# Performance work log

Measured on AMD Instinct MI355X. Metric: run time of the kernel, lower is better.

## Reference

```python
import jax, jax.numpy as jnp
import numpy as np

EPS = 1e-3


def setup_inputs() -> dict:
    key = jax.random.key(0)
    k1, k2 = jax.random.split(key)
    U, N, C_in, C_out = 40000, 32, 9, 64
    inputs = jax.random.normal(k1, (U, N, C_in), dtype=jnp.float32)
    # torch nn.Linear weight has shape (out, in)
    W = jax.random.normal(k2, (C_out, C_in), dtype=jnp.float32) * (1.0 / np.sqrt(C_in))
    gamma = jnp.ones((C_out,), dtype=jnp.float32)
    beta = jnp.zeros((C_out,), dtype=jnp.float32)
    return {"inputs": inputs, "W": W, "gamma": gamma, "beta": beta}


def reference(inputs, W, gamma, beta):
    # Linear (no bias): (U, N, C_in) x (C_out, C_in) -> (U, N, C_out)
    x = jnp.einsum('unc,oc->uno', inputs, W)
    # BatchNorm1d in training mode: stats over batch and points dims (U, N),
    # biased variance, as torch uses for normalization.
    mean = jnp.mean(x, axis=(0, 1))            # (C_out,)
    var = jnp.var(x, axis=(0, 1))              # (C_out,) biased
    x = (x - mean) * jax.lax.rsqrt(var + EPS) * gamma + beta
    x = jax.nn.relu(x)
    # Max over points dim, keepdim -> (U, 1, C_out)
    return jnp.max(x, axis=1, keepdims=True)
```

## Files before the change

kernel.cpp:

```cpp
#include <hip/hip_runtime.h>
#include <math.h>

#define U_TOTAL 40000
#define N_PTS   32
#define C_IN    9
#define C_OUT   64
#define UPB     8
#define NBLK_A  (U_TOTAL / UPB)
#define EPSV    1e-3f

typedef float  f32x2  __attribute__((ext_vector_type(2)));
typedef float  f32x16 __attribute__((ext_vector_type(16)));
typedef short  short8 __attribute__((ext_vector_type(8)));

__device__ __forceinline__ void gl_lds16(const void* g, void* l) {
    __builtin_amdgcn_global_load_lds(
        (const __attribute__((address_space(1))) unsigned int*)g,
        (__attribute__((address_space(3))) unsigned int*)l, 16, 0, 0);
}

__device__ __forceinline__ unsigned pk_bf16(float lo, float hi) {
    unsigned r;
    asm("v_cvt_pk_bf16_f32 %0, %1, %2" : "=v"(r) : "v"(lo), "v"(hi));
    return r;
}

__global__ __launch_bounds__(256, 4)
void pfn_a(const float* __restrict__ in, const float* __restrict__ Wg,
           float* __restrict__ out, float* __restrict__ partials)
{
    __shared__ __align__(16) float lbuf[UPB * N_PTS * C_IN];
    __shared__ float red[4][2][64];

    const int tid  = threadIdx.x;
    const int lane = tid & 63;
    const int w    = tid >> 6;
    const int col  = lane & 31;
    const int g    = lane >> 5;

    unsigned b0[4], b1[4];
    {
        const float* wr0 = Wg + (size_t)col * C_IN + g * 4;
        const float* wr1 = Wg + (size_t)(32 + col) * C_IN + g * 4;
        float a0 = wr0[0], a1 = wr0[1], a2 = wr0[2], a3 = wr0[3];
        float c0 = wr1[0], c1 = wr1[1], c2 = wr1[2], c3 = wr1[3];
        float k8a = g ? 0.f : Wg[(size_t)col * C_IN + 8];
        float k8c = g ? 0.f : Wg[(size_t)(32 + col) * C_IN + 8];
        b0[0] = pk_bf16(a0, a1); b0[1] = pk_bf16(a2, a3);
        b0[2] = pk_bf16(k8a, 0.f); b0[3] = 0u;
        b1[0] = pk_bf16(c0, c1); b1[1] = pk_bf16(c2, c3);
        b1[2] = pk_bf16(k8c, 0.f); b1[3] = 0u;
    }
    union { unsigned u[4]; short8 v; } B0, B1;
    B0.u[0]=b0[0]; B0.u[1]=b0[1]; B0.u[2]=b0[2]; B0.u[3]=b0[3];
    B1.u[0]=b1[0]; B1.u[1]=b1[1]; B1.u[2]=b1[2]; B1.u[3]=b1[3];

    const char* gt = (const char*)in + (size_t)blockIdx.x * (UPB * N_PTS * C_IN * 4);
    {
        int s0 = tid;
        gl_lds16(gt + s0 * 16, (char*)lbuf + (s0 & ~63) * 16);
        int s1 = 256 + tid;
        gl_lds16(gt + s1 * 16, (char*)lbuf + (s1 & ~63) * 16);
        if (tid < 64) {
            int s2 = 512 + tid;
            gl_lds16(gt + s2 * 16, (char*)lbuf + (s2 & ~63) * 16);
        }
    }
    __syncthreads();

    f32x2 S1_0 = {0.f,0.f}, S2_0 = {0.f,0.f}, S1_1 = {0.f,0.f}, S2_1 = {0.f,0.f};
    const int u0 = blockIdx.x * UPB;

#pragma unroll
    for (int t = 0; t < 2; ++t) {
        const int uloc = 2 * w + t;
        const int r    = uloc * N_PTS + col;
        const float* rp = lbuf + (size_t)r * C_IN;

        float f0 = rp[g * 4 + 0], f1 = rp[g * 4 + 1];
        float f2 = rp[g * 4 + 2], f3 = rp[g * 4 + 3];
        float f4 = rp[g ? 4 : 8];
        f4 = g ? 0.f : f4;
        union { unsigned u[4]; short8 v; } A;
        A.u[0] = pk_bf16(f0, f1);
        A.u[1] = pk_bf16(f2, f3);
        A.u[2] = pk_bf16(f4, 0.f);
        A.u[3] = 0u;

        f32x16 z = {};
        f32x16 d0 = __builtin_amdgcn_mfma_f32_32x32x16_bf16(A.v, B0.v, z, 0, 0, 0);
        f32x16 d1 = __builtin_amdgcn_mfma_f32_32x32x16_bf16(A.v, B1.v, z, 0, 0, 0);

        union { f32x16 v; f32x2 p[8]; } D0, D1;
        D0.v = d0; D1.v = d1;
        f32x2 mx0 = D0.p[0], mx1 = D1.p[0];
#pragma unroll
        for (int i = 0; i < 8; ++i) {
            S1_0 += D0.p[i];
            S2_0 = __builtin_elementwise_fma(D0.p[i], D0.p[i], S2_0);
            S1_1 += D1.p[i];
            S2_1 = __builtin_elementwise_fma(D1.p[i], D1.p[i], S2_1);
            if (i) {
                mx0 = __builtin_elementwise_max(mx0, D0.p[i]);
                mx1 = __builtin_elementwise_max(mx1, D1.p[i]);
            }
        }
        float m0 = fmaxf(mx0.x, mx0.y);
        float m1 = fmaxf(mx1.x, mx1.y);
        m0 = fmaxf(m0, __shfl_xor(m0, 32));
        m1 = fmaxf(m1, __shfl_xor(m1, 32));
        out[(size_t)(u0 + uloc) * C_OUT + lane] = g ? m1 : m0;
    }

    float s1_0 = S1_0.x + S1_0.y, s2_0 = S2_0.x + S2_0.y;
    float s1_1 = S1_1.x + S1_1.y, s2_1 = S2_1.x + S2_1.y;
    s1_0 += __shfl_xor(s1_0, 32);
    s2_0 += __shfl_xor(s2_0, 32);
    s1_1 += __shfl_xor(s1_1, 32);
    s2_1 += __shfl_xor(s2_1, 32);
    if (g == 0) {
        red[w][0][col]      = s1_0;
        red[w][0][32 + col] = s1_1;
        red[w][1][col]      = s2_0;
        red[w][1][32 + col] = s2_1;
    }
    __syncthreads();
    if (tid < 128) {
        const int o = tid >> 1, k = tid & 1;
        float acc = red[0][k][o] + red[1][k][o] + red[2][k][o] + red[3][k][o];
        partials[(size_t)blockIdx.x * 128 + tid] = acc;
    }
}

__global__ __launch_bounds__(256)
void pfn_reduce(const float* __restrict__ partials, float* __restrict__ sums, int nblocks)
{
    const int b = blockIdx.x;
    const int t = threadIdx.x;
    float acc = 0.f;
    for (int i = t; i < nblocks; i += 256) acc += partials[(size_t)i * 128 + b];
    __shared__ float r[256];
    r[t] = acc;
    __syncthreads();
    for (int s = 128; s > 0; s >>= 1) {
        if (t < s) r[t] += r[t + s];
        __syncthreads();
    }
    if (t == 0) sums[b] = r[0];
}

__global__ __launch_bounds__(256)
void pfn_c(float* __restrict__ out, const float* __restrict__ sums,
           const float* __restrict__ gamma, const float* __restrict__ beta)
{
    const int idx = blockIdx.x * 256 + threadIdx.x;
    const int o = (idx & 15) * 4;
    const float invM = 1.0f / (float)(U_TOTAL * N_PTS);
    float4 v   = ((const float4*)out)[idx];
    float4 s01 = ((const float4*)sums)[(2 * o) / 4];
    float4 s23 = ((const float4*)sums)[(2 * o) / 4 + 1];
    float4 g4  = ((const float4*)gamma)[o / 4];
    float4 b4  = ((const float4*)beta)[o / 4];

#define BN1(x, S1, S2, g, b) ({                                   \
        float mean_ = (S1) * invM;                                \
        float var_  = (S2) * invM - mean_ * mean_;                \
        float sc_   = (g) * __frsqrt_rn(var_ + EPSV);             \
        fmaxf(fmaf((x), sc_, (b) - mean_ * sc_), 0.0f); })

    v.x = BN1(v.x, s01.x, s01.y, g4.x, b4.x);
    v.y = BN1(v.y, s01.z, s01.w, g4.y, b4.y);
    v.z = BN1(v.z, s23.x, s23.y, g4.z, b4.z);
    v.w = BN1(v.w, s23.z, s23.w, g4.w, b4.w);
#undef BN1
    ((float4*)out)[idx] = v;
}

extern "C" void kernel_launch(void* const* d_in, const int* in_sizes, int n_in,
                              void* d_out, int out_size, void* d_ws, size_t ws_size,
                              hipStream_t stream)
{
    const float* in    = (const float*)d_in[0];
    const float* Wg    = (const float*)d_in[1];
    const float* gamma = (const float*)d_in[2];
    const float* beta  = (const float*)d_in[3];
    float* out = (float*)d_out;

    float* partials = (float*)d_ws;
    float* sums     = partials + (size_t)NBLK_A * 128;

    pfn_a<<<NBLK_A, 256, 0, stream>>>(in, Wg, out, partials);
    pfn_reduce<<<128, 256, 0, stream>>>(partials, sums, NBLK_A);
    pfn_c<<<(U_TOTAL * C_OUT / 4) / 256, 256, 0, stream>>>(out, sums, gamma, beta);
}
```

Baseline: 31.92 us.

## Double-buffer input chunks per block and transpose partials layout for coalesced reduce

Each block now processes four 8-unit chunks, staging them into two LDS buffers with async global-to-LDS loads, so loading the next chunk overlaps compute on the current one. Blocks drop from 5000 to 1250, which cuts per-block weight setup and partial count. The partials array is transposed so the reduce kernel reads contiguous addresses. The cost is explicit vmcnt waits and barriers per chunk, plus less block-level parallelism to hide latency.

```diff
diff --git a/kernel.cpp b/kernel.cpp
--- a/kernel.cpp
+++ b/kernel.cpp
@@ -5,8 +5,11 @@
 #define N_PTS   32
 #define C_IN    9
 #define C_OUT   64
-#define UPB     8
+#define UPC     8
+#define CPB     4
+#define UPB     (UPC * CPB)
 #define NBLK_A  (U_TOTAL / UPB)
+#define CHUNK_BYTES (UPC * N_PTS * C_IN * 4)
 #define EPSV    1e-3f
 
 typedef float  f32x2  __attribute__((ext_vector_type(2)));
@@ -25,11 +28,24 @@
     return r;
 }
 
+#define WAITV(N) asm volatile("s_waitcnt vmcnt(" #N ")" ::: "memory")
+
+__device__ __forceinline__ void stage_chunk(const char* __restrict__ src,
+                                            char* dst, int tid) {
+    if (tid < 192) {
+#pragma unroll
+        for (int i = 0; i < 3; ++i) {
+            const int slot = i * 192 + tid;
+            gl_lds16(src + slot * 16, dst + (slot & ~63) * 16);
+        }
+    }
+}
+
 __global__ __launch_bounds__(256, 4)
 void pfn_a(const float* __restrict__ in, const float* __restrict__ Wg,
            float* __restrict__ out, float* __restrict__ partials)
 {
-    __shared__ __align__(16) float lbuf[UPB * N_PTS * C_IN];
+    __shared__ __align__(16) float lbuf[2][UPC * N_PTS * C_IN];
     __shared__ float red[4][2][64];
 
     const int tid  = threadIdx.x;
@@ -38,7 +54,13 @@
     const int col  = lane & 31;
     const int g    = lane >> 5;
 
-    unsigned b0[4], b1[4];
+    const char* gtile = (const char*)in + (size_t)blockIdx.x * (CPB * CHUNK_BYTES);
+
+    stage_chunk(gtile + 0 * CHUNK_BYTES, (char*)lbuf[0], tid);
+    stage_chunk(gtile + 1 * CHUNK_BYTES, (char*)lbuf[1], tid);
+    __builtin_amdgcn_sched_barrier(0);
+
+    union { unsigned u[4]; short8 v; } B0, B1;
     {
         const float* wr0 = Wg + (size_t)col * C_IN + g * 4;
         const float* wr1 = Wg + (size_t)(32 + col) * C_IN + g * 4;
@@ -46,70 +68,68 @@
         float c0 = wr1[0], c1 = wr1[1], c2 = wr1[2], c3 = wr1[3];
         float k8a = g ? 0.f : Wg[(size_t)col * C_IN + 8];
         float k8c = g ? 0.f : Wg[(size_t)(32 + col) * C_IN + 8];
-        b0[0] = pk_bf16(a0, a1); b0[1] = pk_bf16(a2, a3);
-        b0[2] = pk_bf16(k8a, 0.f); b0[3] = 0u;
-        b1[0] = pk_bf16(c0, c1); b1[1] = pk_bf16(c2, c3);
-        b1[2] = pk_bf16(k8c, 0.f); b1[3] = 0u;
-    }
-    union { unsigned u[4]; short8 v; } B0, B1;
-    B0.u[0]=b0[0]; B0.u[1]=b0[1]; B0.u[2]=b0[2]; B0.u[3]=b0[3];
-    B1.u[0]=b1[0]; B1.u[1]=b1[1]; B1.u[2]=b1[2]; B1.u[3]=b1[3];
-
-    const char* gt = (const char*)in + (size_t)blockIdx.x * (UPB * N_PTS * C_IN * 4);
-    {
-        int s0 = tid;
-        gl_lds16(gt + s0 * 16, (char*)lbuf + (s0 & ~63) * 16);
-        int s1 = 256 + tid;
-        gl_lds16(gt + s1 * 16, (char*)lbuf + (s1 & ~63) * 16);
-        if (tid < 64) {
-            int s2 = 512 + tid;
-            gl_lds16(gt + s2 * 16, (char*)lbuf + (s2 & ~63) * 16);
-        }
-    }
-    __syncthreads();
+        B0.u[0] = pk_bf16(a0, a1);  B0.u[1] = pk_bf16(a2, a3);
+        B0.u[2] = pk_bf16(k8a, 0.f); B0.u[3] = 0u;
+        B1.u[0] = pk_bf16(c0, c1);  B1.u[1] = pk_bf16(c2, c3);
+        B1.u[2] = pk_bf16(k8c, 0.f); B1.u[3] = 0u;
+    }
 
     f32x2 S1_0 = {0.f,0.f}, S2_0 = {0.f,0.f}, S1_1 = {0.f,0.f}, S2_1 = {0.f,0.f};
     const int u0 = blockIdx.x * UPB;
 
 #pragma unroll
-    for (int t = 0; t < 2; ++t) {
-        const int uloc = 2 * w + t;
-        const int r    = uloc * N_PTS + col;
-        const float* rp = lbuf + (size_t)r * C_IN;
-
-        float f0 = rp[g * 4 + 0], f1 = rp[g * 4 + 1];
-        float f2 = rp[g * 4 + 2], f3 = rp[g * 4 + 3];
-        float f4 = rp[g ? 4 : 8];
-        f4 = g ? 0.f : f4;
-        union { unsigned u[4]; short8 v; } A;
-        A.u[0] = pk_bf16(f0, f1);
-        A.u[1] = pk_bf16(f2, f3);
-        A.u[2] = pk_bf16(f4, 0.f);
-        A.u[3] = 0u;
-
-        f32x16 z = {};
-        f32x16 d0 = __builtin_amdgcn_mfma_f32_32x32x16_bf16(A.v, B0.v, z, 0, 0, 0);
-        f32x16 d1 = __builtin_amdgcn_mfma_f32_32x32x16_bf16(A.v, B1.v, z, 0, 0, 0);
-
-        union { f32x16 v; f32x2 p[8]; } D0, D1;
-        D0.v = d0; D1.v = d1;
-        f32x2 mx0 = D0.p[0], mx1 = D1.p[0];
-#pragma unroll
-        for (int i = 0; i < 8; ++i) {
-            S1_0 += D0.p[i];
-            S2_0 = __builtin_elementwise_fma(D0.p[i], D0.p[i], S2_0);
-            S1_1 += D1.p[i];
-            S2_1 = __builtin_elementwise_fma(D1.p[i], D1.p[i], S2_1);
-            if (i) {
-                mx0 = __builtin_elementwise_max(mx0, D0.p[i]);
-                mx1 = __builtin_elementwise_max(mx1, D1.p[i]);
+    for (int c = 0; c < CPB; ++c) {
+        if (c < CPB - 1) { if (w < 3) WAITV(3); }
+        else             { WAITV(0); }
+        __builtin_amdgcn_s_barrier();
+        __builtin_amdgcn_sched_barrier(0);
+
+        const float* lb = lbuf[c & 1];
+#pragma unroll
+        for (int t = 0; t < 2; ++t) {
+            const int uloc = 2 * w + t;
+            const float* rp = lb + (size_t)(uloc * N_PTS + col) * C_IN;
+
+            float f0 = rp[g * 4 + 0], f1 = rp[g * 4 + 1];
+            float f2 = rp[g * 4 + 2], f3 = rp[g * 4 + 3];
+            float f4 = rp[g ? 4 : 8];
+            f4 = g ? 0.f : f4;
+            union { unsigned u[4]; short8 v; } A;
+            A.u[0] = pk_bf16(f0, f1);
+            A.u[1] = pk_bf16(f2, f3);
+            A.u[2] = pk_bf16(f4, 0.f);
+            A.u[3] = 0u;
+
+            f32x16 z = {};
+            f32x16 d0 = __builtin_amdgcn_mfma_f32_32x32x16_bf16(A.v, B0.v, z, 0, 0, 0);
+            f32x16 d1 = __builtin_amdgcn_mfma_f32_32x32x16_bf16(A.v, B1.v, z, 0, 0, 0);
+
+            union { f32x16 v; f32x2 p[8]; } D0, D1;
+            D0.v = d0; D1.v = d1;
+            f32x2 mx0 = D0.p[0], mx1 = D1.p[0];
+#pragma unroll
+            for (int i = 0; i < 8; ++i) {
+                S1_0 += D0.p[i];
+                S2_0 = __builtin_elementwise_fma(D0.p[i], D0.p[i], S2_0);
+                S1_1 += D1.p[i];
+                S2_1 = __builtin_elementwise_fma(D1.p[i], D1.p[i], S2_1);
+                if (i) {
+                    mx0 = __builtin_elementwise_max(mx0, D0.p[i]);
+                    mx1 = __builtin_elementwise_max(mx1, D1.p[i]);
+                }
             }
+            float m0 = fmaxf(mx0.x, mx0.y);
+            float m1 = fmaxf(mx1.x, mx1.y);
+            m0 = fmaxf(m0, __shfl_xor(m0, 32));
+            m1 = fmaxf(m1, __shfl_xor(m1, 32));
+            out[(size_t)(u0 + c * UPC + uloc) * C_OUT + lane] = g ? m1 : m0;
         }
-        float m0 = fmaxf(mx0.x, mx0.y);
-        float m1 = fmaxf(mx1.x, mx1.y);
-        m0 = fmaxf(m0, __shfl_xor(m0, 32));
-        m1 = fmaxf(m1, __shfl_xor(m1, 32));
-        out[(size_t)(u0 + uloc) * C_OUT + lane] = g ? m1 : m0;
+
+        __builtin_amdgcn_sched_barrier(0);
+        __builtin_amdgcn_s_barrier();
+        if (c + 2 < CPB)
+            stage_chunk(gtile + (c + 2) * CHUNK_BYTES, (char*)lbuf[c & 1], tid);
+        __builtin_amdgcn_sched_barrier(0);
     }
 
     float s1_0 = S1_0.x + S1_0.y, s2_0 = S2_0.x + S2_0.y;
@@ -128,7 +148,7 @@
     if (tid < 128) {
         const int o = tid >> 1, k = tid & 1;
         float acc = red[0][k][o] + red[1][k][o] + red[2][k][o] + red[3][k][o];
-        partials[(size_t)blockIdx.x * 128 + tid] = acc;
+        partials[(size_t)tid * NBLK_A + blockIdx.x] = acc;
     }
 }
 
@@ -138,7 +158,7 @@
     const int b = blockIdx.x;
     const int t = threadIdx.x;
     float acc = 0.f;
-    for (int i = t; i < nblocks; i += 256) acc += partials[(size_t)i * 128 + b];
+    for (int i = t; i < nblocks; i += 256) acc += partials[(size_t)b * nblocks + i];
     __shared__ float r[256];
     r[t] = acc;
     __syncthreads();
@@ -187,7 +207,7 @@
     float* out = (float*)d_out;
 
     float* partials = (float*)d_ws;
-    float* sums     = partials + (size_t)NBLK_A * 128;
+    float* sums     = partials + (size_t)128 * NBLK_A;
 
     pfn_a<<<NBLK_A, 256, 0, stream>>>(in, Wg, out, partials);
     pfn_reduce<<<128, 256, 0, stream>>>(partials, sums, NBLK_A);
```

After: 47.86 us. +49.9%, slower.

## Load inputs directly from global into registers, skipping LDS staging

Applied to the files above, without the earlier changes.

Drops the global-to-LDS async copy and the barrier that followed it. Each lane now reads its point's features straight from global memory with unaligned float4 plus scalar loads. Each wave handles 4 units instead of 2, and the occupancy hint is raised from 4 to 6. This removes the LDS round trip and the block sync, but the direct global loads are strided by 36 bytes and poorly coalesced, and there are half as many blocks.

```diff
diff --git a/kernel.cpp b/kernel.cpp
--- a/kernel.cpp
+++ b/kernel.cpp
@@ -5,19 +5,15 @@
 #define N_PTS   32
 #define C_IN    9
 #define C_OUT   64
-#define UPB     8
+#define UPW     4
+#define UPB     (UPW * 4)
 #define NBLK_A  (U_TOTAL / UPB)
 #define EPSV    1e-3f
 
 typedef float  f32x2  __attribute__((ext_vector_type(2)));
 typedef float  f32x16 __attribute__((ext_vector_type(16)));
 typedef short  short8 __attribute__((ext_vector_type(8)));
-
-__device__ __forceinline__ void gl_lds16(const void* g, void* l) {
-    __builtin_amdgcn_global_load_lds(
-        (const __attribute__((address_space(1))) unsigned int*)g,
-        (__attribute__((address_space(3))) unsigned int*)l, 16, 0, 0);
-}
+typedef float  f32x4u __attribute__((ext_vector_type(4), aligned(4)));
 
 __device__ __forceinline__ unsigned pk_bf16(float lo, float hi) {
     unsigned r;
@@ -25,11 +21,10 @@
     return r;
 }
 
-__global__ __launch_bounds__(256, 4)
+__global__ __launch_bounds__(256, 6)
 void pfn_a(const float* __restrict__ in, const float* __restrict__ Wg,
            float* __restrict__ out, float* __restrict__ partials)
 {
-    __shared__ __align__(16) float lbuf[UPB * N_PTS * C_IN];
     __shared__ float red[4][2][64];
 
     const int tid  = threadIdx.x;
@@ -38,53 +33,37 @@
     const int col  = lane & 31;
     const int g    = lane >> 5;
 
-    unsigned b0[4], b1[4];
-    {
-        const float* wr0 = Wg + (size_t)col * C_IN + g * 4;
-        const float* wr1 = Wg + (size_t)(32 + col) * C_IN + g * 4;
-        float a0 = wr0[0], a1 = wr0[1], a2 = wr0[2], a3 = wr0[3];
-        float c0 = wr1[0], c1 = wr1[1], c2 = wr1[2], c3 = wr1[3];
-        float k8a = g ? 0.f : Wg[(size_t)col * C_IN + 8];
-        float k8c = g ? 0.f : Wg[(size_t)(32 + col) * C_IN + 8];
-        b0[0] = pk_bf16(a0, a1); b0[1] = pk_bf16(a2, a3);
-        b0[2] = pk_bf16(k8a, 0.f); b0[3] = 0u;
-        b1[0] = pk_bf16(c0, c1); b1[1] = pk_bf16(c2, c3);
-        b1[2] = pk_bf16(k8c, 0.f); b1[3] = 0u;
+    const float* wr0 = Wg + (size_t)col * C_IN + g * 4;
+    const float* wr1 = Wg + (size_t)(32 + col) * C_IN + g * 4;
+    float a0 = wr0[0], a1 = wr0[1], a2 = wr0[2], a3 = wr0[3];
+    float c0 = wr1[0], c1 = wr1[1], c2 = wr1[2], c3 = wr1[3];
+    float k8a = g ? 0.f : Wg[(size_t)col * C_IN + 8];
+    float k8c = g ? 0.f : Wg[(size_t)(32 + col) * C_IN + 8];
+    union { unsigned u[4]; short8 v; } B0, B1;
+    B0.u[0] = pk_bf16(a0, a1);  B0.u[1] = pk_bf16(a2, a3);
+    B0.u[2] = pk_bf16(k8a, 0.f); B0.u[3] = 0u;
+    B1.u[0] = pk_bf16(c0, c1);  B1.u[1] = pk_bf16(c2, c3);
+    B1.u[2] = pk_bf16(k8c, 0.f); B1.u[3] = 0u;
+
+    const int u0 = blockIdx.x * UPB + w * UPW;
+    const float* base = in + (size_t)u0 * (N_PTS * C_IN) + col * C_IN;
+    f32x4u q[UPW];
+    float  f8[UPW];
+#pragma unroll
+    for (int t = 0; t < UPW; ++t) {
+        const float* rp = base + t * (N_PTS * C_IN);
+        q[t]  = *(const f32x4u*)(rp + 4 * g);
+        f8[t] = rp[8];
     }
-    union { unsigned u[4]; short8 v; } B0, B1;
-    B0.u[0]=b0[0]; B0.u[1]=b0[1]; B0.u[2]=b0[2]; B0.u[3]=b0[3];
-    B1.u[0]=b1[0]; B1.u[1]=b1[1]; B1.u[2]=b1[2]; B1.u[3]=b1[3];
-
-    const char* gt = (const char*)in + (size_t)blockIdx.x * (UPB * N_PTS * C_IN * 4);
-    {
-        int s0 = tid;
-        gl_lds16(gt + s0 * 16, (char*)lbuf + (s0 & ~63) * 16);
-        int s1 = 256 + tid;
-        gl_lds16(gt + s1 * 16, (char*)lbuf + (s1 & ~63) * 16);
-        if (tid < 64) {
-            int s2 = 512 + tid;
-            gl_lds16(gt + s2 * 16, (char*)lbuf + (s2 & ~63) * 16);
-        }
-    }
-    __syncthreads();
 
     f32x2 S1_0 = {0.f,0.f}, S2_0 = {0.f,0.f}, S1_1 = {0.f,0.f}, S2_1 = {0.f,0.f};
-    const int u0 = blockIdx.x * UPB;
 
 #pragma unroll
-    for (int t = 0; t < 2; ++t) {
-        const int uloc = 2 * w + t;
-        const int r    = uloc * N_PTS + col;
-        const float* rp = lbuf + (size_t)r * C_IN;
-
-        float f0 = rp[g * 4 + 0], f1 = rp[g * 4 + 1];
-        float f2 = rp[g * 4 + 2], f3 = rp[g * 4 + 3];
-        float f4 = rp[g ? 4 : 8];
-        f4 = g ? 0.f : f4;
+    for (int t = 0; t < UPW; ++t) {
         union { unsigned u[4]; short8 v; } A;
-        A.u[0] = pk_bf16(f0, f1);
-        A.u[1] = pk_bf16(f2, f3);
-        A.u[2] = pk_bf16(f4, 0.f);
+        A.u[0] = pk_bf16(q[t].x, q[t].y);
+        A.u[1] = pk_bf16(q[t].z, q[t].w);
+        A.u[2] = pk_bf16(g ? 0.f : f8[t], 0.f);
         A.u[3] = 0u;
 
         f32x16 z = {};
@@ -109,7 +88,7 @@
         float m1 = fmaxf(mx1.x, mx1.y);
         m0 = fmaxf(m0, __shfl_xor(m0, 32));
         m1 = fmaxf(m1, __shfl_xor(m1, 32));
-        out[(size_t)(u0 + uloc) * C_OUT + lane] = g ? m1 : m0;
+        out[(size_t)(u0 + t) * C_OUT + lane] = g ? m1 : m0;
     }
 
     float s1_0 = S1_0.x + S1_0.y, s2_0 = S2_0.x + S2_0.y;
```

New measurement: 27.54 us. 13.7% less time.
